# Kernel optimization log

Measured on AMD Instinct MI355X. Metric: run time of the kernel, lower is better.

Reference implementation:

```python
import jax, jax.numpy as jnp
import numpy as np
import math

B, H, N, DH = 4, 8, 1024, 128
DPT = 4  # point feature dim (<=4 branch: squared-distance map only)

def setup_inputs() -> dict:
    key = jax.random.key(0)
    ks = jax.random.split(key, 10)
    q   = jax.random.normal(ks[0], (B, H, N, DH), jnp.float32)
    k   = jax.random.normal(ks[1], (B, H, N, DH), jnp.float32)
    v   = jax.random.normal(ks[2], (B, H, N, DH), jnp.float32)
    c   = jax.random.normal(ks[3], (B, H, N, 1), jnp.float32)
    d_q = jax.random.normal(ks[4], (B, N, DPT), jnp.float32)
    d_k = jax.random.normal(ks[5], (B, N, DPT), jnp.float32)
    # LazyLinear(1 -> nhead): per-head scalar weight + bias
    w_w = jax.random.normal(ks[6], (H,), jnp.float32) * 0.1
    b_w = jax.random.normal(ks[7], (H,), jnp.float32) * 0.1
    w_b = jax.random.normal(ks[8], (H,), jnp.float32) * 0.1
    b_b = jax.random.normal(ks[9], (H,), jnp.float32) * 0.1
    return {"q": q, "k": k, "v": v, "c": c, "d_q": d_q, "d_k": d_k,
            "w_w": w_w, "b_w": b_w, "w_b": w_b, "b_b": b_b}

def reference(q, k, v, c, d_q, d_k, w_w, b_w, w_b, b_b):
    dh = q.shape[-1]
    # pairwise squared distances on first 3 coords (torch: under no_grad)
    dq3 = d_q[:, :, :3]
    dk3 = d_k[:, :, :3]
    dist = jax.lax.stop_gradient(
        jnp.sum(dq3 ** 2, -1)[:, :, None]
        + jnp.sum(dk3 ** 2, -1)[:, None, :]
        - 2.0 * jnp.einsum('bnd,bmd->bnm', dq3, dk3))  # [B,N,M]
    db = dist[:, None, :, :]  # [B,1,N,M]
    wbc = lambda p: p[None, :, None, None]  # [1,H,1,1]
    # distmap_w = softplus(-(w*dist + b)); distmap_b = w*dist + b (identity acts)
    distmap_w = jax.nn.softplus(-(db * wbc(w_w) + wbc(b_w)))  # [B,H,N,M]
    distmap_b = db * wbc(w_b) + wbc(b_b)                      # [B,H,N,M]
    # scaled dot-product scores per head
    scores = jnp.einsum('bhnd,bhmd->bhnm', q, k) / math.sqrt(dh)
    scores = jax.nn.relu(scores * distmap_w + distmap_b)
    detr = (jnp.sum(scores, -1, keepdims=True)
            + jnp.sum(jax.nn.softplus(c), 2, keepdims=True) + 1e-9)
    scores = scores / detr
    out = jnp.einsum('bhnm,bhmd->bhnd', scores, v)
    return out, scores
```

## Files before the change

### kernel.cpp

```cpp
#include <hip/hip_runtime.h>


typedef __attribute__((ext_vector_type(8))) short short8;
typedef __attribute__((ext_vector_type(4))) float f32x4;

#define OUT_ELEMS 4194304ull
#define WS_K      0ull
#define WS_VT     8388608ull
#define WS_CS     16777216ull

__device__ __forceinline__ unsigned short f2bf(float f) {
    unsigned u = __builtin_bit_cast(unsigned, f);
    u += 0x7FFFu + ((u >> 16) & 1u);
    return (unsigned short)(u >> 16);
}
__device__ __forceinline__ float softplus(float x) {
    return fmaxf(x, 0.f) + __logf(1.f + __expf(-fabsf(x)));
}

__global__ __launch_bounds__(256) void prep_all(
    const float* __restrict__ k, const float* __restrict__ v, const float* __restrict__ c,
    unsigned short* __restrict__ wsK, unsigned short* __restrict__ wsVt, float* __restrict__ wsCs)
{
    __shared__ unsigned short sT[64 * 132];
    const int blk = blockIdx.x, tid = threadIdx.x;
    if (blk < 512) {
        int t = blk * 256 + tid;
        for (int u = t; u < 524288; u += 131072) {
            float4 a = reinterpret_cast<const float4*>(k)[u * 2];
            float4 b = reinterpret_cast<const float4*>(k)[u * 2 + 1];
            short8 o;
            o[0]=(short)f2bf(a.x); o[1]=(short)f2bf(a.y); o[2]=(short)f2bf(a.z); o[3]=(short)f2bf(a.w);
            o[4]=(short)f2bf(b.x); o[5]=(short)f2bf(b.y); o[6]=(short)f2bf(b.z); o[7]=(short)f2bf(b.w);
            reinterpret_cast<short8*>(wsK)[u] = o;
        }
    } else if (blk < 1024) {
        const int vb = blk - 512;
        const int bh = vb >> 4, m0 = (vb & 15) * 64;
        const float* src = v + ((size_t)bh * 1024 + m0) * 128;
        for (int i = tid; i < 2048; i += 256) {
            int row = i >> 5, c4 = i & 31;
            float4 t = reinterpret_cast<const float4*>(src)[i];
            unsigned long long pk = (unsigned long long)f2bf(t.x)
                                  | ((unsigned long long)f2bf(t.y) << 16)
                                  | ((unsigned long long)f2bf(t.z) << 32)
                                  | ((unsigned long long)f2bf(t.w) << 48);
            *reinterpret_cast<unsigned long long*>(&sT[row * 132 + c4 * 4]) = pk;
        }
        __syncthreads();
        for (int u = tid; u < 2048; u += 256) {
            int dh = u >> 4, ms = u & 15;
            unsigned long long pk = (unsigned long long)sT[(ms*4+0)*132 + dh]
                                  | ((unsigned long long)sT[(ms*4+1)*132 + dh] << 16)
                                  | ((unsigned long long)sT[(ms*4+2)*132 + dh] << 32)
                                  | ((unsigned long long)sT[(ms*4+3)*132 + dh] << 48);
            *reinterpret_cast<unsigned long long*>(&wsVt[((size_t)bh * 128 + dh) * 1024 + m0 + ms * 4]) = pk;
        }
    } else {
        __shared__ float red[4];
        const int bh = blk - 1024;
        float p = 0.f;
        for (int i = tid; i < 1024; i += 256) p += softplus(c[(size_t)bh * 1024 + i]);
        p += __shfl_xor(p, 32, 64); p += __shfl_xor(p, 16, 64); p += __shfl_xor(p, 8, 64);
        p += __shfl_xor(p,  4, 64); p += __shfl_xor(p,  2, 64); p += __shfl_xor(p, 1, 64);
        if ((tid & 63) == 0) red[tid >> 6] = p;
        __syncthreads();
        if (tid == 0) wsCs[bh] = red[0] + red[1] + red[2] + red[3] + 1e-9f;
    }
}

__global__ __launch_bounds__(512, 4) void sam_main(
    const float* __restrict__ q, const float* __restrict__ dqp, const float* __restrict__ dkp,
    const float* __restrict__ w_w, const float* __restrict__ b_w,
    const float* __restrict__ w_b, const float* __restrict__ b_b,
    const unsigned short* __restrict__ wsK, const unsigned short* __restrict__ wsVt,
    const float* __restrict__ wsCs, float* __restrict__ out)
{
    __shared__ __align__(16) unsigned short sKall[2 * 8704];
    __shared__ __align__(16) unsigned short sVtall[2 * 9216];
    __shared__ float sdkall[2 * 256];
    __shared__ float s_inv[64];

    const int bid  = blockIdx.x;
    const int bh   = bid & 31;
    const int n0   = (bid >> 5) * 64;
    const int b    = bh >> 3;
    const int h    = bh & 7;
    const int tid  = threadIdx.x;
    const int lane = tid & 63;
    const int wave = tid >> 6;
    const int g    = wave >> 2;
    const int wl   = wave & 3;
    const int w16  = wl * 16;
    const int tg   = tid & 255;
    const int l15  = lane & 15;
    const int quad = lane >> 4;

    const float ww = w_w[h], bw = b_w[h], wb = w_b[h], bb = b_b[h];
    const float SCALE = 0.08838834764831845f;

    {
        const float* qbase = q + ((size_t)bh * 1024 + n0) * 128;
        for (int i = tid; i < 2048; i += 512) {
            int row = i >> 5, c4 = i & 31;
            float4 t = reinterpret_cast<const float4*>(qbase)[i];
            unsigned long long pk = (unsigned long long)f2bf(t.x)
                                  | ((unsigned long long)f2bf(t.y) << 16)
                                  | ((unsigned long long)f2bf(t.z) << 32)
                                  | ((unsigned long long)f2bf(t.w) << 48);
            *reinterpret_cast<unsigned long long*>(&sKall[row * 136 + c4 * 4]) = pk;
        }
    }
    float qx[4], qy[4], qz[4], qs[4];
    #pragma unroll
    for (int r = 0; r < 4; r++) {
        int nl = w16 + quad * 4 + r;
        float4 d4 = reinterpret_cast<const float4*>(dqp)[(size_t)b * 1024 + n0 + nl];
        qx[r] = d4.x; qy[r] = d4.y; qz[r] = d4.z;
        qs[r] = d4.x*d4.x + d4.y*d4.y + d4.z*d4.z;
    }
    const float cs = wsCs[bh];
    __syncthreads();
    short8 afr[4];
    {
        const unsigned short* aq = &sKall[(w16 + l15) * 136];
        #pragma unroll
        for (int ks = 0; ks < 4; ks++)
            afr[ks] = *reinterpret_cast<const short8*>(aq + ks * 32 + quad * 8);
    }
    __syncthreads();

    unsigned short* sKg  = sKall  + g * 8704;
    unsigned short* sVtg = sVtall + g * 9216;
    unsigned short* sP   = sKg + wl * 1152;
    float* sdkg = sdkall + g * 256;

    float rs[4] = {0.f, 0.f, 0.f, 0.f};
    for (int t8 = 0; t8 < 8; t8++) {
        const int m0 = (t8 * 2 + g) * 64;
        for (int i = tg; i < 1024; i += 256) {
            int row = i >> 4, seg = i & 15;
            short8 d = *reinterpret_cast<const short8*>(wsK + ((size_t)bh * 1024 + m0 + row) * 128 + seg * 8);
            *reinterpret_cast<short8*>(&sKg[row * 136 + seg * 8]) = d;
        }
        if (tg < 64) {
            float4 d4 = reinterpret_cast<const float4*>(dkp)[(size_t)b * 1024 + m0 + tg];
            sdkg[tg] = d4.x; sdkg[64 + tg] = d4.y; sdkg[128 + tg] = d4.z;
            sdkg[192 + tg] = d4.x*d4.x + d4.y*d4.y + d4.z*d4.z;
        }
        __syncthreads();

        f32x4 cacc[4];
        #pragma unroll
        for (int mf = 0; mf < 4; mf++) {
            cacc[mf] = {0.f, 0.f, 0.f, 0.f};
            const unsigned short* bq = &sKg[(mf * 16 + l15) * 136];
            #pragma unroll
            for (int ks = 0; ks < 4; ks++) {
                short8 bfr = *reinterpret_cast<const short8*>(bq + ks * 32 + quad * 8);
                cacc[mf] = __builtin_amdgcn_mfma_f32_16x16x32_bf16(afr[ks], bfr, cacc[mf], 0, 0, 0);
            }
        }
        #pragma unroll
        for (int mf = 0; mf < 4; mf++) {
            const int mloc = mf * 16 + l15;
            const float kx = sdkg[mloc], ky = sdkg[64 + mloc], kz = sdkg[128 + mloc], ksq = sdkg[192 + mloc];
            #pragma unroll
            for (int r = 0; r < 4; r++) {
                float dist = qs[r] + ksq - 2.f * (qx[r]*kx + qy[r]*ky + qz[r]*kz);
                float aw = softplus(-(dist * ww + bw));
                float ab = dist * wb + bb;
                rs[r] += fmaxf(cacc[mf][r] * SCALE * aw + ab, 0.f);
            }
        }
        __syncthreads();
    }

    #pragma unroll
    for (int r = 0; r < 4; r++) {
        float t = rs[r];
        t += __shfl_xor(t, 1, 64); t += __shfl_xor(t, 2, 64);
        t += __shfl_xor(t, 4, 64); t += __shfl_xor(t, 8, 64);
        if (l15 == 0) sdkall[g * 256 + w16 + quad * 4 + r] = t;
    }
    __syncthreads();
    if (tid < 64) s_inv[tid] = 1.f / (sdkall[tid] + sdkall[256 + tid] + cs);
    __syncthreads();

    float inv4[4];
    #pragma unroll
    for (int r = 0; r < 4; r++) inv4[r] = s_inv[w16 + quad * 4 + r];

    f32x4 oacc[8];
    #pragma unroll
    for (int i = 0; i < 8; i++) oacc[i] = {0.f, 0.f, 0.f, 0.f};
    float* scb = out + OUT_ELEMS + ((size_t)bh << 20);

    for (int t8 = 0; t8 < 8; t8++) {
        const int m0 = (t8 * 2 + g) * 64;
        for (int i = tg; i < 1024; i += 256) {
            int row = i >> 4, seg = i & 15;
            short8 d = *reinterpret_cast<const short8*>(wsK + ((size_t)bh * 1024 + m0 + row) * 128 + seg * 8);
            *reinterpret_cast<short8*>(&sKg[row * 136 + seg * 8]) = d;
        }
        for (int i = tg; i < 1024; i += 256) {
            int dh = i >> 3, seg = i & 7;
            short8 d = *reinterpret_cast<const short8*>(wsVt + ((size_t)bh * 128 + dh) * 1024 + m0 + seg * 8);
            *reinterpret_cast<short8*>(&sVtg[dh * 72 + seg * 8]) = d;
        }
        if (tg < 64) {
            float4 d4 = reinterpret_cast<const float4*>(dkp)[(size_t)b * 1024 + m0 + tg];
            sdkg[tg] = d4.x; sdkg[64 + tg] = d4.y; sdkg[128 + tg] = d4.z;
            sdkg[192 + tg] = d4.x*d4.x + d4.y*d4.y + d4.z*d4.z;
        }
        __syncthreads();

        f32x4 cacc[4];
        #pragma unroll
        for (int mf = 0; mf < 4; mf++) {
            cacc[mf] = {0.f, 0.f, 0.f, 0.f};
            const unsigned short* bq = &sKg[(mf * 16 + l15) * 136];
            #pragma unroll
            for (int ks = 0; ks < 4; ks++) {
                short8 bfr = *reinterpret_cast<const short8*>(bq + ks * 32 + quad * 8);
                cacc[mf] = __builtin_amdgcn_mfma_f32_16x16x32_bf16(afr[ks], bfr, cacc[mf], 0, 0, 0);
            }
        }
        __syncthreads();

        #pragma unroll
        for (int mf = 0; mf < 4; mf++) {
            const int mloc = mf * 16 + l15;
            const float kx = sdkg[mloc], ky = sdkg[64 + mloc], kz = sdkg[128 + mloc], ksq = sdkg[192 + mloc];
            #pragma unroll
            for (int r = 0; r < 4; r++) {
                float dist = qs[r] + ksq - 2.f * (qx[r]*kx + qy[r]*ky + qz[r]*kz);
                float aw = softplus(-(dist * ww + bw));
                float ab = dist * wb + bb;
                float val = fmaxf(cacc[mf][r] * SCALE * aw + ab, 0.f);
                float p   = val * inv4[r];
                sP[(quad * 4 + r) * 72 + mf * 16 + l15] = f2bf(p);
                scb[(size_t)(n0 + w16 + quad * 4 + r) * 1024 + m0 + mf * 16 + l15] = p;
            }
        }
        #pragma unroll
        for (int ks2 = 0; ks2 < 2; ks2++) {
            short8 pfr = *reinterpret_cast<const short8*>(&sP[l15 * 72 + ks2 * 32 + quad * 8]);
            #pragma unroll
            for (int df = 0; df < 8; df++) {
                short8 vfr = *reinterpret_cast<const short8*>(&sVtg[(df * 16 + l15) * 72 + ks2 * 32 + quad * 8]);
                oacc[df] = __builtin_amdgcn_mfma_f32_16x16x32_bf16(pfr, vfr, oacc[df], 0, 0, 0);
            }
        }
        __syncthreads();
    }

    float* sO = reinterpret_cast<float*>(sKall) + wl * 2112;
    if (g == 1) {
        #pragma unroll
        for (int df = 0; df < 8; df++)
            #pragma unroll
            for (int r = 0; r < 4; r++)
                sO[(quad * 4 + r) * 132 + df * 16 + l15] = oacc[df][r];
    }
    __syncthreads();
    if (g == 0) {
        #pragma unroll
        for (int df = 0; df < 8; df++) {
            #pragma unroll
            for (int r = 0; r < 4; r++) {
                int row = w16 + quad * 4 + r;
                float o = oacc[df][r] + sO[(quad * 4 + r) * 132 + df * 16 + l15];
                out[((size_t)bh * 1024 + n0 + row) * 128 + df * 16 + l15] = o;
            }
        }
    }
}

extern "C" void kernel_launch(void* const* d_in, const int* in_sizes, int n_in,
                              void* d_out, int out_size, void* d_ws, size_t ws_size,
                              hipStream_t stream) {
    const float* q   = (const float*)d_in[0];
    const float* k   = (const float*)d_in[1];
    const float* v   = (const float*)d_in[2];
    const float* c   = (const float*)d_in[3];
    const float* dq  = (const float*)d_in[4];
    const float* dk  = (const float*)d_in[5];
    const float* w_w = (const float*)d_in[6];
    const float* b_w = (const float*)d_in[7];
    const float* w_b = (const float*)d_in[8];
    const float* b_b = (const float*)d_in[9];
    float* out = (float*)d_out;
    char* ws = (char*)d_ws;
    unsigned short* wsK  = (unsigned short*)(ws + WS_K);
    unsigned short* wsVt = (unsigned short*)(ws + WS_VT);
    float* wsCs   = (float*)(ws + WS_CS);

    hipLaunchKernelGGL(prep_all, dim3(1056), dim3(256), 0, stream, k, v, c, wsK, wsVt, wsCs);
    hipLaunchKernelGGL(sam_main, dim3(512), dim3(512), 0, stream,
                       q, dq, dk, w_w, b_w, w_b, b_b, wsK, wsVt, wsCs, out);
}
```

Baseline: 269.3 us.

## Cache unnormalized scores in registers to skip recomputing QK^T in second pass

New measurement: 273.4 us. No clear change (+1.5%).

```diff
diff --git a/kernel.cpp b/kernel.cpp
--- a/kernel.cpp
+++ b/kernel.cpp
@@ -16,6 +16,11 @@
 }
 __device__ __forceinline__ float softplus(float x) {
     return fmaxf(x, 0.f) + __logf(1.f + __expf(-fabsf(x)));
+}
+__device__ __forceinline__ unsigned cvt_pk_bf16(float lo, float hi) {
+    unsigned r;
+    asm("v_cvt_pk_bf16_f32 %0, %1, %2" : "=v"(r) : "v"(lo), "v"(hi));
+    return r;
 }
 
 __global__ __launch_bounds__(256) void prep_all(
@@ -76,204 +81,174 @@
     const unsigned short* __restrict__ wsK, const unsigned short* __restrict__ wsVt,
     const float* __restrict__ wsCs, float* __restrict__ out)
 {
-    __shared__ __align__(16) unsigned short sKall[2 * 8704];
-    __shared__ __align__(16) unsigned short sVtall[2 * 9216];
-    __shared__ float sdkall[2 * 256];
-    __shared__ float s_inv[64];
+    __shared__ __align__(16) unsigned short sK[64 * 136];
+    __shared__ __align__(16) unsigned short sVt[128 * 72];
+    __shared__ __align__(16) unsigned short sP[32 * 72];
+    __shared__ float sdk[4 * 64];
+    __shared__ float s_red[4 * 32];
+    __shared__ float s_inv[32];
 
     const int bid  = blockIdx.x;
-    const int bh   = bid & 31;
-    const int n0   = (bid >> 5) * 64;
+    const int xcd  = bid & 7;
+    const int j    = bid >> 3;
+    const int bh   = xcd * 4 + (j & 3);
+    const int n0   = (j >> 2) * 32;
     const int b    = bh >> 3;
     const int h    = bh & 7;
     const int tid  = threadIdx.x;
     const int lane = tid & 63;
     const int wave = tid >> 6;
-    const int g    = wave >> 2;
-    const int wl   = wave & 3;
-    const int w16  = wl * 16;
-    const int tg   = tid & 255;
     const int l15  = lane & 15;
     const int quad = lane >> 4;
+    const int wr   = wave >> 2;
+    const int wc   = wave & 3;
+    const int mq   = wc * 16 + l15;
 
     const float ww = w_w[h], bw = b_w[h], wb = w_b[h], bb = b_b[h];
+    const float wwn = -ww, bwn = -bw;
     const float SCALE = 0.08838834764831845f;
 
+    unsigned short* sQ = sVt;
     {
         const float* qbase = q + ((size_t)bh * 1024 + n0) * 128;
-        for (int i = tid; i < 2048; i += 512) {
+        for (int i = tid; i < 1024; i += 512) {
             int row = i >> 5, c4 = i & 31;
             float4 t = reinterpret_cast<const float4*>(qbase)[i];
-            unsigned long long pk = (unsigned long long)f2bf(t.x)
-                                  | ((unsigned long long)f2bf(t.y) << 16)
-                                  | ((unsigned long long)f2bf(t.z) << 32)
-                                  | ((unsigned long long)f2bf(t.w) << 48);
-            *reinterpret_cast<unsigned long long*>(&sKall[row * 136 + c4 * 4]) = pk;
-        }
-    }
-    float qx[4], qy[4], qz[4], qs[4];
+            unsigned long long pk = (unsigned long long)f2bf(t.x * SCALE)
+                                  | ((unsigned long long)f2bf(t.y * SCALE) << 16)
+                                  | ((unsigned long long)f2bf(t.z * SCALE) << 32)
+                                  | ((unsigned long long)f2bf(t.w * SCALE) << 48);
+            *reinterpret_cast<unsigned long long*>(&sQ[row * 136 + c4 * 4]) = pk;
+        }
+    }
+    float qxm[4], qym[4], qzm[4], qs[4];
     #pragma unroll
     for (int r = 0; r < 4; r++) {
-        int nl = w16 + quad * 4 + r;
+        int nl = wr * 16 + quad * 4 + r;
         float4 d4 = reinterpret_cast<const float4*>(dqp)[(size_t)b * 1024 + n0 + nl];
-        qx[r] = d4.x; qy[r] = d4.y; qz[r] = d4.z;
+        qxm[r] = -2.f * d4.x; qym[r] = -2.f * d4.y; qzm[r] = -2.f * d4.z;
         qs[r] = d4.x*d4.x + d4.y*d4.y + d4.z*d4.z;
     }
     const float cs = wsCs[bh];
     __syncthreads();
     short8 afr[4];
     {
-        const unsigned short* aq = &sKall[(w16 + l15) * 136];
+        const unsigned short* aq = &sQ[(wr * 16 + l15) * 136];
         #pragma unroll
         for (int ks = 0; ks < 4; ks++)
             afr[ks] = *reinterpret_cast<const short8*>(aq + ks * 32 + quad * 8);
     }
     __syncthreads();
 
-    unsigned short* sKg  = sKall  + g * 8704;
-    unsigned short* sVtg = sVtall + g * 9216;
-    unsigned short* sP   = sKg + wl * 1152;
-    float* sdkg = sdkall + g * 256;
-
     float rs[4] = {0.f, 0.f, 0.f, 0.f};
-    for (int t8 = 0; t8 < 8; t8++) {
-        const int m0 = (t8 * 2 + g) * 64;
-        for (int i = tg; i < 1024; i += 256) {
-            int row = i >> 4, seg = i & 15;
+    unsigned vreg[16][2];
+    #pragma unroll
+    for (int t = 0; t < 16; t++) {
+        const int m0 = t * 64;
+        #pragma unroll
+        for (int i = 0; i < 2; i++) {
+            int u = tid + i * 512;
+            int row = u >> 4, seg = u & 15;
             short8 d = *reinterpret_cast<const short8*>(wsK + ((size_t)bh * 1024 + m0 + row) * 128 + seg * 8);
-            *reinterpret_cast<short8*>(&sKg[row * 136 + seg * 8]) = d;
-        }
-        if (tg < 64) {
-            float4 d4 = reinterpret_cast<const float4*>(dkp)[(size_t)b * 1024 + m0 + tg];
-            sdkg[tg] = d4.x; sdkg[64 + tg] = d4.y; sdkg[128 + tg] = d4.z;
-            sdkg[192 + tg] = d4.x*d4.x + d4.y*d4.y + d4.z*d4.z;
-        }
-        __syncthreads();
-
-        f32x4 cacc[4];
-        #pragma unroll
-        for (int mf = 0; mf < 4; mf++) {
-            cacc[mf] = {0.f, 0.f, 0.f, 0.f};
-            const unsigned short* bq = &sKg[(mf * 16 + l15) * 136];
+            *reinterpret_cast<short8*>(&sK[row * 136 + seg * 8]) = d;
+        }
+        if (tid < 64) {
+            float4 d4 = reinterpret_cast<const float4*>(dkp)[(size_t)b * 1024 + m0 + tid];
+            sdk[tid] = d4.x; sdk[64 + tid] = d4.y; sdk[128 + tid] = d4.z;
+            sdk[192 + tid] = d4.x*d4.x + d4.y*d4.y + d4.z*d4.z;
+        }
+        __syncthreads();
+
+        f32x4 cacc = {0.f, 0.f, 0.f, 0.f};
+        {
+            const unsigned short* bq = &sK[(wc * 16 + l15) * 136];
             #pragma unroll
             for (int ks = 0; ks < 4; ks++) {
                 short8 bfr = *reinterpret_cast<const short8*>(bq + ks * 32 + quad * 8);
-                cacc[mf] = __builtin_amdgcn_mfma_f32_16x16x32_bf16(afr[ks], bfr, cacc[mf], 0, 0, 0);
+                cacc = __builtin_amdgcn_mfma_f32_16x16x32_bf16(afr[ks], bfr, cacc, 0, 0, 0);
             }
         }
-        #pragma unroll
-        for (int mf = 0; mf < 4; mf++) {
-            const int mloc = mf * 16 + l15;
-            const float kx = sdkg[mloc], ky = sdkg[64 + mloc], kz = sdkg[128 + mloc], ksq = sdkg[192 + mloc];
+        const float kx = sdk[mq], ky = sdk[64 + mq], kz = sdk[128 + mq], ksq = sdk[192 + mq];
+        float val[4];
+        #pragma unroll
+        for (int r = 0; r < 4; r++) {
+            float dist = qs[r] + ksq + qxm[r]*kx + qym[r]*ky + qzm[r]*kz;
+            float aw = softplus(dist * wwn + bwn);
+            float ab = dist * wb + bb;
+            val[r] = fmaxf(cacc[r] * aw + ab, 0.f);
+            rs[r] += val[r];
+        }
+        vreg[t][0] = cvt_pk_bf16(val[0], val[1]);
+        vreg[t][1] = cvt_pk_bf16(val[2], val[3]);
+        __syncthreads();
+    }
+
+    #pragma unroll
+    for (int r = 0; r < 4; r++) {
+        float tsum = rs[r];
+        tsum += __shfl_xor(tsum, 1, 64);
+        tsum += __shfl_xor(tsum, 2, 64);
+        tsum += __shfl_xor(tsum, 4, 64);
+        tsum += __shfl_xor(tsum, 8, 64);
+        if (l15 == 0) s_red[wc * 32 + wr * 16 + quad * 4 + r] = tsum;
+    }
+    __syncthreads();
+    if (tid < 32) s_inv[tid] = 1.f / (s_red[tid] + s_red[32 + tid] + s_red[64 + tid] + s_red[96 + tid] + cs);
+    __syncthreads();
+    float inv4[4];
+    #pragma unroll
+    for (int r = 0; r < 4; r++) inv4[r] = s_inv[wr * 16 + quad * 4 + r];
+
+    f32x4 oacc[2];
+    oacc[0] = {0.f, 0.f, 0.f, 0.f};
+    oacc[1] = {0.f, 0.f, 0.f, 0.f};
+    float* scb = out + OUT_ELEMS + ((size_t)bh << 20)
+               + (size_t)(n0 + wr * 16 + quad * 4) * 1024 + mq;
+
+    #pragma unroll
+    for (int t = 0; t < 16; t++) {
+        const int m0 = t * 64;
+        #pragma unroll
+        for (int i = 0; i < 2; i++) {
+            int u = tid + i * 512;
+            int dh = u >> 3, seg = u & 7;
+            short8 d = *reinterpret_cast<const short8*>(wsVt + ((size_t)bh * 128 + dh) * 1024 + m0 + seg * 8);
+            *reinterpret_cast<short8*>(&sVt[dh * 72 + seg * 8]) = d;
+        }
+        {
+            unsigned pv0 = vreg[t][0], pv1 = vreg[t][1];
+            unsigned short vb0 = (unsigned short)pv0, vb1 = (unsigned short)(pv0 >> 16);
+            unsigned short vb2 = (unsigned short)pv1, vb3 = (unsigned short)(pv1 >> 16);
+            unsigned short* pbase = &sP[(wr * 16 + quad * 4) * 72 + mq];
+            pbase[0]   = vb0;
+            pbase[72]  = vb1;
+            pbase[144] = vb2;
+            pbase[216] = vb3;
+            scb[m0]        = __builtin_bit_cast(float, (unsigned)vb0 << 16) * inv4[0];
+            scb[m0 + 1024] = __builtin_bit_cast(float, (unsigned)vb1 << 16) * inv4[1];
+            scb[m0 + 2048] = __builtin_bit_cast(float, (unsigned)vb2 << 16) * inv4[2];
+            scb[m0 + 3072] = __builtin_bit_cast(float, (unsigned)vb3 << 16) * inv4[3];
+        }
+        __syncthreads();
+        #pragma unroll
+        for (int ks2 = 0; ks2 < 2; ks2++) {
+            short8 pfr = *reinterpret_cast<const short8*>(&sP[(wr * 16 + l15) * 72 + ks2 * 32 + quad * 8]);
             #pragma unroll
-            for (int r = 0; r < 4; r++) {
-                float dist = qs[r] + ksq - 2.f * (qx[r]*kx + qy[r]*ky + qz[r]*kz);
-                float aw = softplus(-(dist * ww + bw));
-                float ab = dist * wb + bb;
-                rs[r] += fmaxf(cacc[mf][r] * SCALE * aw + ab, 0.f);
-            }
-        }
-        __syncthreads();
-    }
-
-    #pragma unroll
-    for (int r = 0; r < 4; r++) {
-        float t = rs[r];
-        t += __shfl_xor(t, 1, 64); t += __shfl_xor(t, 2, 64);
-        t += __shfl_xor(t, 4, 64); t += __shfl_xor(t, 8, 64);
-        if (l15 == 0) sdkall[g * 256 + w16 + quad * 4 + r] = t;
-    }
-    __syncthreads();
-    if (tid < 64) s_inv[tid] = 1.f / (sdkall[tid] + sdkall[256 + tid] + cs);
-    __syncthreads();
-
-    float inv4[4];
-    #pragma unroll
-    for (int r = 0; r < 4; r++) inv4[r] = s_inv[w16 + quad * 4 + r];
-
-    f32x4 oacc[8];
-    #pragma unroll
-    for (int i = 0; i < 8; i++) oacc[i] = {0.f, 0.f, 0.f, 0.f};
-    float* scb = out + OUT_ELEMS + ((size_t)bh << 20);
-
-    for (int t8 = 0; t8 < 8; t8++) {
-        const int m0 = (t8 * 2 + g) * 64;
-        for (int i = tg; i < 1024; i += 256) {
-            int row = i >> 4, seg = i & 15;
-            short8 d = *reinterpret_cast<const short8*>(wsK + ((size_t)bh * 1024 + m0 + row) * 128 + seg * 8);
-            *reinterpret_cast<short8*>(&sKg[row * 136 + seg * 8]) = d;
-        }
-        for (int i = tg; i < 1024; i += 256) {
-            int dh = i >> 3, seg = i & 7;
-            short8 d = *reinterpret_cast<const short8*>(wsVt + ((size_t)bh * 128 + dh) * 1024 + m0 + seg * 8);
-            *reinterpret_cast<short8*>(&sVtg[dh * 72 + seg * 8]) = d;
-        }
-        if (tg < 64) {
-            float4 d4 = reinterpret_cast<const float4*>(dkp)[(size_t)b * 1024 + m0 + tg];
-            sdkg[tg] = d4.x; sdkg[64 + tg] = d4.y; sdkg[128 + tg] = d4.z;
-            sdkg[192 + tg] = d4.x*d4.x + d4.y*d4.y + d4.z*d4.z;
-        }
-        __syncthreads();
-
-        f32x4 cacc[4];
-        #pragma unroll
-        for (int mf = 0; mf < 4; mf++) {
-            cacc[mf] = {0.f, 0.f, 0.f, 0.f};
-            const unsigned short* bq = &sKg[(mf * 16 + l15) * 136];
-            #pragma unroll
-            for (int ks = 0; ks < 4; ks++) {
-                short8 bfr = *reinterpret_cast<const short8*>(bq + ks * 32 + quad * 8);
-                cacc[mf] = __builtin_amdgcn_mfma_f32_16x16x32_bf16(afr[ks], bfr, cacc[mf], 0, 0, 0);
-            }
-        }
-        __syncthreads();
-
-        #pragma unroll
-        for (int mf = 0; mf < 4; mf++) {
-            const int mloc = mf * 16 + l15;
-            const float kx = sdkg[mloc], ky = sdkg[64 + mloc], kz = sdkg[128 + mloc], ksq = sdkg[192 + mloc];
-            #pragma unroll
-            for (int r = 0; r < 4; r++) {
-                float dist = qs[r] + ksq - 2.f * (qx[r]*kx + qy[r]*ky + qz[r]*kz);
-                float aw = softplus(-(dist * ww + bw));
-                float ab = dist * wb + bb;
-                float val = fmaxf(cacc[mf][r] * SCALE * aw + ab, 0.f);
-                float p   = val * inv4[r];
-                sP[(quad * 4 + r) * 72 + mf * 16 + l15] = f2bf(p);
-                scb[(size_t)(n0 + w16 + quad * 4 + r) * 1024 + m0 + mf * 16 + l15] = p;
-            }
-        }
-        #pragma unroll
-        for (int ks2 = 0; ks2 < 2; ks2++) {
-            short8 pfr = *reinterpret_cast<const short8*>(&sP[l15 * 72 + ks2 * 32 + quad * 8]);
-            #pragma unroll
-            for (int df = 0; df < 8; df++) {
-                short8 vfr = *reinterpret_cast<const short8*>(&sVtg[(df * 16 + l15) * 72 + ks2 * 32 + quad * 8]);
+            for (int df = 0; df < 2; df++) {
+                short8 vfr = *reinterpret_cast<const short8*>(&sVt[(wc * 32 + df * 16 + l15) * 72 + ks2 * 32 + quad * 8]);
                 oacc[df] = __builtin_amdgcn_mfma_f32_16x16x32_bf16(pfr, vfr, oacc[df], 0, 0, 0);
             }
         }
         __syncthreads();
     }
 
-    float* sO = reinterpret_cast<float*>(sKall) + wl * 2112;
-    if (g == 1) {
-        #pragma unroll
-        for (int df = 0; df < 8; df++)
+    {
+        float* obase = out + ((size_t)bh * 1024 + n0 + wr * 16 + quad * 4) * 128 + wc * 32 + l15;
+        #pragma unroll
+        for (int df = 0; df < 2; df++)
             #pragma unroll
             for (int r = 0; r < 4; r++)
-                sO[(quad * 4 + r) * 132 + df * 16 + l15] = oacc[df][r];
-    }
-    __syncthreads();
-    if (g == 0) {
-        #pragma unroll
-        for (int df = 0; df < 8; df++) {
-            #pragma unroll
-            for (int r = 0; r < 4; r++) {
-                int row = w16 + quad * 4 + r;
-                float o = oacc[df][r] + sO[(quad * 4 + r) * 132 + df * 16 + l15];
-                out[((size_t)bh * 1024 + n0 + row) * 128 + df * 16 + l15] = o;
-            }
-        }
+                obase[(size_t)r * 128 + df * 16] = oacc[df][r] * inv4[r];
     }
 }
 
@@ -297,6 +272,6 @@
     float* wsCs   = (float*)(ws + WS_CS);
 
     hipLaunchKernelGGL(prep_all, dim3(1056), dim3(256), 0, stream, k, v, c, wsK, wsVt, wsCs);
-    hipLaunchKernelGGL(sam_main, dim3(512), dim3(512), 0, stream,
+    hipLaunchKernelGGL(sam_main, dim3(1024), dim3(512), 0, stream,
                        q, dq, dk, w_w, b_w, w_b, b_b, wsK, wsVt, wsCs, out);
 }
```
